# Optimization experiments

Hardware: AMD Instinct MI355X
Metric: run time of the kernel (lower is better)

Reference implementation:

```python
import jax, jax.numpy as jnp
import numpy as np

B, S, D, H, L, V, DF = 2, 1024, 1024, 16, 4, 32000, 4096


def setup_inputs() -> dict:
    key = jax.random.key(0)
    ks = iter(jax.random.split(key, 64))
    rn = lambda shape, s=0.02: jax.random.normal(next(ks), shape, jnp.float32) * s
    inp = {
        'dec_input': rn((B, S, D), 1.0),
        'enc_input': rn((B, S, D), 1.0),
        # additive masks: causal for self-attn, none for cross-attn
        'masked_attention_mask': jnp.where(jnp.tril(jnp.ones((S, S), bool)), 0.0, -1e9)[None, None].astype(jnp.float32),
        'cross_attention_mask': jnp.zeros((1, 1, S, S), jnp.float32),
        'num_heads': H,
    }
    for p in ['sWq', 'sWk', 'sWv', 'sWo', 'cWq', 'cWk', 'cWv', 'cWo']:
        inp[p] = rn((L, D, D))
    for p in ['sbq', 'sbk', 'sbv', 'sbo', 'cbq', 'cbk', 'cbv', 'cbo']:
        inp[p] = jnp.zeros((L, D), jnp.float32)
    for p in ['ln1_g', 'ln2_g', 'ln3_g']:
        inp[p] = jnp.ones((L, D), jnp.float32)
    for p in ['ln1_b', 'ln2_b', 'ln3_b']:
        inp[p] = jnp.zeros((L, D), jnp.float32)
    inp['fW1'] = rn((L, D, DF)); inp['fb1'] = jnp.zeros((L, DF), jnp.float32)
    inp['fW2'] = rn((L, DF, D)); inp['fb2'] = jnp.zeros((L, D), jnp.float32)
    inp['Wout'] = rn((D, V)); inp['bout'] = jnp.zeros((V,), jnp.float32)
    return inp


def positional_encoding(seq_len, d_model, n=10000.0):
    # vectorized equivalent of the original triple-nested loop:
    # even d -> sin(i / n^(d/D)); odd d -> cos(i / n^((d-1)/D)); d==0 denom 1 == n^0
    i = jnp.arange(seq_len, dtype=jnp.float32)[:, None]
    d = jnp.arange(d_model)
    denom = jnp.power(n, (2 * (d // 2)).astype(jnp.float32) / d_model)
    ang = i / denom
    return jnp.where(d % 2 == 0, jnp.sin(ang), jnp.cos(ang))  # [S, D]


def layer_norm(x, g, b, eps=1e-5):
    m = jnp.mean(x, -1, keepdims=True)
    v = jnp.mean(jnp.square(x - m), -1, keepdims=True)
    return (x - m) * jax.lax.rsqrt(v + eps) * g + b


def mha(q_in, k_in, v_in, mask, Wq, bq, Wk, bk, Wv, bv, Wo, bo, h):
    b, sq, d = q_in.shape
    dh = d // h
    q = (q_in @ Wq + bq).reshape(b, sq, h, dh)
    k = (k_in @ Wk + bk).reshape(b, -1, h, dh)
    v = (v_in @ Wv + bv).reshape(b, -1, h, dh)
    scores = jnp.einsum('bqhd,bkhd->bhqk', q, k) / jnp.sqrt(jnp.float32(dh)) + mask
    attn = jax.nn.softmax(scores, axis=-1)
    out = jnp.einsum('bhqk,bkhd->bqhd', attn, v).reshape(b, sq, d)
    return out @ Wo + bo


def reference(dec_input, enc_input, masked_attention_mask, cross_attention_mask,
              sWq, sbq, sWk, sbk, sWv, sbv, sWo, sbo,
              cWq, cbq, cWk, cbk, cWv, cbv, cWo, cbo,
              ln1_g, ln1_b, ln2_g, ln2_b, ln3_g, ln3_b,
              fW1, fb1, fW2, fb2, Wout, bout, num_heads):
    b, s, d = dec_input.shape
    x0 = dec_input + positional_encoding(s, d)
    n_layers = sWq.shape[0]
    y = x0
    for l in range(n_layers):
        # NOTE: original DecoderSequential bug: every block consumes the ORIGINAL input;
        # only the last block's output survives.
        a1 = layer_norm(x0 + mha(x0, x0, x0, masked_attention_mask,
                                 sWq[l], sbq[l], sWk[l], sbk[l], sWv[l], sbv[l], sWo[l], sbo[l], num_heads),
                        ln1_g[l], ln1_b[l])
        a2 = layer_norm(a1 + mha(a1, enc_input, enc_input, cross_attention_mask,
                                 cWq[l], cbq[l], cWk[l], cbk[l], cWv[l], cbv[l], cWo[l], cbo[l], num_heads),
                        ln2_g[l], ln2_b[l])
        ff = jax.nn.relu(a2 @ fW1[l] + fb1[l]) @ fW2[l] + fb2[l]
        y = layer_norm(a2 + ff, ln3_g[l], ln3_b[l])
    return y @ Wout + bout  # [B, S, V]
```

## Files before the change

### kernel.cpp

```cpp
#include <hip/hip_runtime.h>
#include <cstdint>
#include <cstddef>

#define DEV __device__ __forceinline__

typedef __attribute__((ext_vector_type(8))) short short8;
typedef __attribute__((ext_vector_type(4))) float f32x4;
typedef __attribute__((ext_vector_type(16))) float f32x16;
typedef __attribute__((ext_vector_type(4))) unsigned short ushort4v;

DEV unsigned short f2bf(float f){
  union { float f; unsigned int i; } v; v.f = f;
  unsigned int r = v.i + 0x7fffu + ((v.i >> 16) & 1u);
  return (unsigned short)(r >> 16);
}

DEV void gld_lds16(const unsigned short* g, unsigned short* lds){
  __builtin_amdgcn_global_load_lds((const __attribute__((address_space(1))) void*)g,
                                   (__attribute__((address_space(3))) void*)lds, 16, 0, 0);
}

DEV int swz(int r, int s){
  int ln = r >> 1;
  int sl = ((r & 1) << 2) | s;
  return ln * 64 + (((sl ^ (ln & 7))) << 3);
}

template<int BN, int EPI>
__global__ __launch_bounds__(256, 2)
void gemm32(const unsigned short* __restrict__ A,
            const unsigned short* __restrict__ Bt,
            const float* __restrict__ bias,
            void* __restrict__ C, int M, int N, int K)
{
  constexpr int NFR  = BN / 64;
  constexpr int ROWS = 128 + BN;
  constexpr int BUFH = ROWS * 32;
  constexpr int GLD  = ROWS / 64;
  __shared__ __align__(16) unsigned short lds[3 * BUFH];

  const int tid = threadIdx.x, wid = tid >> 6, l = tid & 63;
  const int wr = wid >> 1, wcn = wid & 1;

  const int nbm = M / 128, nbn = N / BN;
  const int nwg = nbm * nbn;
  const int q8 = nwg >> 3, r8 = nwg & 7;
  const int xcd = blockIdx.x & 7, within = blockIdx.x >> 3;
  const int wg = (xcd < r8 ? xcd * (q8 + 1) : r8 * (q8 + 1) + (xcd - r8) * q8) + within;
  const int mb = (wg % nbm) * 128, nb = (wg / nbm) * BN;

  const int nk = K / 32;

  const int sL   = tid >> 3;
  const int sSl  = (tid & 7) ^ (sL & 7);
  const int sRow = sL * 2 + (sSl >> 2);
  const int sKc  = (sSl & 3) * 8;

  const int r31 = l & 31, hi = l >> 5;

  int aoff[2][2], boff[NFR][2];
  #pragma unroll
  for (int m = 0; m < 2; m++)
    #pragma unroll
    for (int ks = 0; ks < 2; ks++)
      aoff[m][ks] = wr * 2048 + swz(m * 32 + r31, 2 * ks + hi);
  #pragma unroll
  for (int n = 0; n < NFR; n++){
    const int col = wcn * (BN / 2) + n * 32 + r31;
    #pragma unroll
    for (int ks = 0; ks < 2; ks++)
      boff[n][ks] = 4096 + (col >> 6) * 2048 + swz(col & 63, 2 * ks + hi);
  }

  f32x16 acc[2][NFR];
  #pragma unroll
  for (int m = 0; m < 2; m++)
    #pragma unroll
    for (int n = 0; n < NFR; n++)
      #pragma unroll
      for (int e = 0; e < 16; e++) acc[m][n][e] = 0.f;

#define STAGE_A(c, tt, b2) \
  gld_lds16(A + (size_t)(mb + (c)*64 + sRow) * K + (size_t)(tt)*32 + sKc, \
            lds + (b2)*BUFH + (c)*2048 + tid*8)
#define STAGE_B(c, tt, b2) \
  gld_lds16(Bt + (size_t)(nb + (c)*64 + sRow) * K + (size_t)(tt)*32 + sKc, \
            lds + (b2)*BUFH + 4096 + (c)*2048 + tid*8)
#define WAIT_GLD() do { if constexpr (GLD == 6) asm volatile("s_waitcnt vmcnt(6)" ::: "memory"); \
                        else if constexpr (GLD == 4) asm volatile("s_waitcnt vmcnt(4)" ::: "memory"); \
                        else asm volatile("s_waitcnt vmcnt(3)" ::: "memory"); } while(0)

  STAGE_A(0, 0, 0); STAGE_A(1, 0, 0);
  #pragma unroll
  for (int c = 0; c < NFR; c++) STAGE_B(c, 0, 0);
  if (nk > 1){
    STAGE_A(0, 1, 1); STAGE_A(1, 1, 1);
    #pragma unroll
    for (int c = 0; c < NFR; c++) STAGE_B(c, 1, 1);
    WAIT_GLD();
  } else {
    asm volatile("s_waitcnt vmcnt(0)" ::: "memory");
  }
  asm volatile("" ::: "memory");
  __builtin_amdgcn_s_barrier();
  asm volatile("" ::: "memory");

  int bb = 0;
  for (int u = 0; u < nk; u++){
    const unsigned short* buf = lds + bb * BUFH;
    const int sb = (bb >= 1) ? bb - 1 : 2;
    const bool st = (u + 2 < nk);
    short8 af[2], bf[NFR];

    af[0] = *(const short8*)(buf + aoff[0][0]);
    af[1] = *(const short8*)(buf + aoff[1][0]);
    #pragma unroll
    for (int n = 0; n < NFR; n++) bf[n] = *(const short8*)(buf + boff[n][0]);
    if (st){
      STAGE_A(0, u + 2, sb); STAGE_A(1, u + 2, sb);
      if constexpr (NFR == 4) STAGE_B(0, u + 2, sb);
    }
    __builtin_amdgcn_s_setprio(1);
    #pragma unroll
    for (int m = 0; m < 2; m++)
      #pragma unroll
      for (int n = 0; n < NFR; n++)
        acc[m][n] = __builtin_amdgcn_mfma_f32_32x32x16_bf16(af[m], bf[n], acc[m][n], 0, 0, 0);
    __builtin_amdgcn_s_setprio(0);

    af[0] = *(const short8*)(buf + aoff[0][1]);
    af[1] = *(const short8*)(buf + aoff[1][1]);
    #pragma unroll
    for (int n = 0; n < NFR; n++) bf[n] = *(const short8*)(buf + boff[n][1]);
    if (st){
      if constexpr (NFR == 4){ STAGE_B(1, u + 2, sb); STAGE_B(2, u + 2, sb); STAGE_B(3, u + 2, sb); }
      else if constexpr (NFR == 2){ STAGE_B(0, u + 2, sb); STAGE_B(1, u + 2, sb); }
      else { STAGE_B(0, u + 2, sb); }
    }
    __builtin_amdgcn_s_setprio(1);
    #pragma unroll
    for (int m = 0; m < 2; m++)
      #pragma unroll
      for (int n = 0; n < NFR; n++)
        acc[m][n] = __builtin_amdgcn_mfma_f32_32x32x16_bf16(af[m], bf[n], acc[m][n], 0, 0, 0);
    __builtin_amdgcn_s_setprio(0);

    if (st)               WAIT_GLD();
    else if (u + 1 < nk)  asm volatile("s_waitcnt vmcnt(0)" ::: "memory");
    asm volatile("" ::: "memory");
    __builtin_amdgcn_s_barrier();
    asm volatile("" ::: "memory");
    bb = (bb == 2) ? 0 : bb + 1;
  }
#undef WAIT_GLD
#undef STAGE_A
#undef STAGE_B

  #pragma unroll
  for (int n = 0; n < NFR; n++){
    const int col = nb + wcn * (BN / 2) + n * 32 + r31;
    const float bv = bias ? bias[col] : 0.f;
    #pragma unroll
    for (int m = 0; m < 2; m++){
      const int rowb = mb + wr * 64 + m * 32 + 4 * hi;
      #pragma unroll
      for (int reg = 0; reg < 16; reg++){
        const int row = rowb + (reg & 3) + 8 * (reg >> 2);
        float v = acc[m][n][reg] + bv;
        size_t idx = (size_t)row * N + col;
        if (EPI == 0)       ((float*)C)[idx] = v;
        else if (EPI == 3)  __builtin_nontemporal_store(v, &((float*)C)[idx]);
        else if (EPI == 1)  ((unsigned short*)C)[idx] = f2bf(v);
        else { v = v > 0.f ? v : 0.f; ((unsigned short*)C)[idx] = f2bf(v); }
      }
    }
  }
}

template<int CAUSAL>
__global__ __launch_bounds__(256)
void attn_kernel(const unsigned short* __restrict__ Qb, int ldq,
                 const unsigned short* __restrict__ Kb, int ldk,
                 const unsigned short* __restrict__ Vb, int ldv,
                 unsigned short* __restrict__ Ob, int ldo)
{
  constexpr int S = 1024;
  __shared__ __align__(16) unsigned short klds[2][4096];
  __shared__ __align__(16) unsigned short vlds[2][4096];
  __shared__ __align__(16) unsigned short plds[4][16][72];

  const int tid = threadIdx.x, w = tid >> 6, l = tid & 63;
  const int qt = blockIdx.x, bh = blockIdx.y;
  const int b = bh >> 4, h = bh & 15;
  const int hoff = h * 64;
  const size_t rb = (size_t)b * S;

  const int qrow = qt * 64 + w * 16 + (l & 15);
  const unsigned short* qp = Qb + (rb + qrow) * ldq + hoff + ((l >> 4) * 8);
  short8 qf0 = *(const short8*)qp;
  short8 qf1 = *(const short8*)(qp + 32);

  float m_run[4] = {-1e30f, -1e30f, -1e30f, -1e30f};
  float l_run[4] = {0.f, 0.f, 0.f, 0.f};
  f32x4 oacc[4];
  #pragma unroll
  for (int t = 0; t < 4; t++) oacc[t] = (f32x4){0.f, 0.f, 0.f, 0.f};

  const int nkv = CAUSAL ? (qt + 1) : (S / 64);

  const int sRowK  = tid >> 3;
  const int sSlotK = (tid & 7) ^ ((tid >> 3) & 7);
  const int skey   = tid >> 3;
  const int sd8    = (tid & 7) * 8;

  int koff[4][2];
  #pragma unroll
  for (int g = 0; g < 4; g++)
    #pragma unroll
    for (int hh = 0; hh < 2; hh++)
      koff[g][hh] = (16 * g + (l & 15)) * 64 + (((hh * 4 + (l >> 4)) ^ (l & 7)) << 3);

  const int vpar = (l >> 3) & 1;
  int voff[4][2];
  #pragma unroll
  for (int t = 0; t < 4; t++)
    #pragma unroll
    for (int ks = 0; ks < 2; ks++)
      voff[t][ks] = (16 * t + (l & 15)) * 64 +
                    ((((ks * 4 + (l >> 4)) ^ (l & 7) ^ ((2 * t + vpar) & 7))) << 3);

#define STAGE_K(c, kt, bf) \
  gld_lds16(Kb + (rb + (size_t)(kt) * 64 + (c) * 32 + sRowK) * ldk + hoff + sSlotK * 8, \
            &klds[bf][(c) * 2048 + tid * 8])
#define LOAD_V(kt, r0v, r1v) do { \
  r0v = *(const short8*)(Vb + (rb + (size_t)(kt) * 64 + skey) * ldv + hoff + sd8); \
  r1v = *(const short8*)(Vb + (rb + (size_t)(kt) * 64 + 32 + skey) * ldv + hoff + sd8); } while(0)
#define WRITE_VT(bf, p, vv) do { \
  _Pragma("unroll") \
  for (int i = 0; i < 8; i++){ \
    vlds[bf][(sd8 + i) * 64 + (((w + 4 * (p)) ^ i ^ (l & 7)) << 3) + (l >> 3)] = \
      (unsigned short)(vv)[i]; \
  } } while(0)

  short8 v0, v1;
  STAGE_K(0, 0, 0); STAGE_K(1, 0, 0);
  LOAD_V(0, v0, v1);
  asm volatile("s_waitcnt vmcnt(0)" ::: "memory");
  WRITE_VT(0, 0, v0); WRITE_VT(0, 1, v1);
  __syncthreads();

  for (int u = 0; u < nkv; u++){
    const int cur = u & 1, nxt = cur ^ 1;
    const bool pre = (u + 1 < nkv);
    if (pre){ STAGE_K(0, u + 1, nxt); STAGE_K(1, u + 1, nxt); LOAD_V(u + 1, v0, v1); }

    f32x4 sc[4];
    #pragma unroll
    for (int g = 0; g < 4; g++){
      short8 k0 = *(const short8*)&klds[cur][koff[g][0]];
      short8 k1 = *(const short8*)&klds[cur][koff[g][1]];
      f32x4 z = (f32x4){0.f, 0.f, 0.f, 0.f};
      z = __builtin_amdgcn_mfma_f32_16x16x32_bf16(qf0, k0, z, 0, 0, 0);
      z = __builtin_amdgcn_mfma_f32_16x16x32_bf16(qf1, k1, z, 0, 0, 0);
      sc[g] = z;
    }

    const bool diag = CAUSAL && (u == qt);
    const int kb = u * 64;
    #pragma unroll
    for (int jj = 0; jj < 4; jj++){
      float s0 = sc[0][jj] * 0.125f, s1 = sc[1][jj] * 0.125f;
      float s2 = sc[2][jj] * 0.125f, s3 = sc[3][jj] * 0.125f;
      if (diag){
        const int q = qt * 64 + w * 16 + ((l >> 4) << 2) + jj;
        const int ky = kb + (l & 15);
        if (ky      > q) s0 = -1e30f;
        if (ky + 16 > q) s1 = -1e30f;
        if (ky + 32 > q) s2 = -1e30f;
        if (ky + 48 > q) s3 = -1e30f;
      }
      float mx = fmaxf(fmaxf(s0, s1), fmaxf(s2, s3));
      mx = fmaxf(mx, __shfl_xor(mx, 1));
      mx = fmaxf(mx, __shfl_xor(mx, 2));
      mx = fmaxf(mx, __shfl_xor(mx, 4));
      mx = fmaxf(mx, __shfl_xor(mx, 8));
      float mnew = fmaxf(m_run[jj], mx);
      float scal = __expf(m_run[jj] - mnew);
      m_run[jj] = mnew;
      float p0 = __expf(s0 - mnew), p1 = __expf(s1 - mnew);
      float p2 = __expf(s2 - mnew), p3 = __expf(s3 - mnew);
      float rs = (p0 + p1) + (p2 + p3);
      rs += __shfl_xor(rs, 1); rs += __shfl_xor(rs, 2);
      rs += __shfl_xor(rs, 4); rs += __shfl_xor(rs, 8);
      l_run[jj] = l_run[jj] * scal + rs;
      #pragma unroll
      for (int t = 0; t < 4; t++) oacc[t][jj] *= scal;
      const int qr = ((l >> 4) << 2) + jj;
      plds[w][qr][l & 15]        = f2bf(p0);
      plds[w][qr][16 + (l & 15)] = f2bf(p1);
      plds[w][qr][32 + (l & 15)] = f2bf(p2);
      plds[w][qr][48 + (l & 15)] = f2bf(p3);
    }
    asm volatile("s_waitcnt lgkmcnt(0)" ::: "memory");
    __builtin_amdgcn_sched_barrier(0);

    short8 pf0 = *(const short8*)&plds[w][l & 15][(l >> 4) * 8];
    short8 pf1 = *(const short8*)&plds[w][l & 15][32 + (l >> 4) * 8];
    #pragma unroll
    for (int t = 0; t < 4; t++){
      short8 va = *(const short8*)&vlds[cur][voff[t][0]];
      short8 vb2 = *(const short8*)&vlds[cur][voff[t][1]];
      f32x4 o = oacc[t];
      o = __builtin_amdgcn_mfma_f32_16x16x32_bf16(pf0, va,  o, 0, 0, 0);
      o = __builtin_amdgcn_mfma_f32_16x16x32_bf16(pf1, vb2, o, 0, 0, 0);
      oacc[t] = o;
    }

    if (pre){
      asm volatile("s_waitcnt vmcnt(0)" ::: "memory");
      WRITE_VT(nxt, 0, v0); WRITE_VT(nxt, 1, v1);
    }
    __syncthreads();
  }
#undef WRITE_VT
#undef LOAD_V
#undef STAGE_K

  #pragma unroll
  for (int jj = 0; jj < 4; jj++){
    float inv = 1.f / l_run[jj];
    int q = qt * 64 + w * 16 + ((l >> 4) << 2) + jj;
    #pragma unroll
    for (int t = 0; t < 4; t++)
      Ob[(rb + q) * ldo + hoff + t * 16 + (l & 15)] = f2bf(oacc[t][jj] * inv);
  }
}

__global__ __launch_bounds__(256)
void ln_kernel(const float* __restrict__ x1, const float* __restrict__ x2,
               const float* __restrict__ g, const float* __restrict__ be,
               float* __restrict__ outf, unsigned short* __restrict__ outb)
{
  const int row = blockIdx.x, t = threadIdx.x;
  __shared__ float red[4];
  const float4 v1 = ((const float4*)(x1 + (size_t)row * 1024))[t];
  const float4 v2 = ((const float4*)(x2 + (size_t)row * 1024))[t];
  float x[4] = {v1.x + v2.x, v1.y + v2.y, v1.z + v2.z, v1.w + v2.w};
  float s = x[0] + x[1] + x[2] + x[3];
  for (int o = 1; o < 64; o <<= 1) s += __shfl_xor(s, o);
  const int w = t >> 6, l = t & 63;
  if (l == 0) red[w] = s;
  __syncthreads();
  const float mean = (red[0] + red[1] + red[2] + red[3]) * (1.f / 1024.f);
  float d[4]; float sq = 0.f;
  #pragma unroll
  for (int i = 0; i < 4; i++){ d[i] = x[i] - mean; sq += d[i] * d[i]; }
  __syncthreads();
  for (int o = 1; o < 64; o <<= 1) sq += __shfl_xor(sq, o);
  if (l == 0) red[w] = sq;
  __syncthreads();
  const float var = (red[0] + red[1] + red[2] + red[3]) * (1.f / 1024.f);
  const float inv = rsqrtf(var + 1e-5f);
  const int base = t * 4;
  #pragma unroll
  for (int i = 0; i < 4; i++){
    float o = d[i] * inv * g[base + i] + be[base + i];
    if (outf) outf[(size_t)row * 1024 + base + i] = o;
    outb[(size_t)row * 1024 + base + i] = f2bf(o);
  }
}

__global__ __launch_bounds__(256)
void build_x0(const float* __restrict__ dec, float* __restrict__ xf, unsigned short* __restrict__ xb)
{
  const int i = blockIdx.x * 256 + threadIdx.x;
  const int i4 = i * 4;
  const int d0 = i4 & 1023;
  const int s  = (i4 >> 10) & 1023;
  float4 dv = ((const float4*)dec)[i];
  const float* dvp = (const float*)&dv;
  float o[4];
  #pragma unroll
  for (int j = 0; j < 4; j++){
    int dd = d0 + j;
    float e = (float)(dd & ~1) * (1.f / 1024.f);
    float den = expf(e * 9.210340371976184f);
    float ang = (float)s / den;
    float pe = (dd & 1) ? cosf(ang) : sinf(ang);
    o[j] = dvp[j] + pe;
  }
  ((float4*)xf)[i] = make_float4(o[0], o[1], o[2], o[3]);
  ushort4v ob; ob[0] = f2bf(o[0]); ob[1] = f2bf(o[1]); ob[2] = f2bf(o[2]); ob[3] = f2bf(o[3]);
  ((ushort4v*)xb)[i] = ob;
}

__global__ __launch_bounds__(256)
void cvt_bf16_k(const float* __restrict__ in, unsigned short* __restrict__ out)
{
  const int i = blockIdx.x * 256 + threadIdx.x;
  float4 v = ((const float4*)in)[i];
  ushort4v o; o[0] = f2bf(v.x); o[1] = f2bf(v.y); o[2] = f2bf(v.z); o[3] = f2bf(v.w);
  ((ushort4v*)out)[i] = o;
}

__global__ __launch_bounds__(256)
void transpose_cvt(const float* __restrict__ in, unsigned short* __restrict__ out, int R, int C)
{
  __shared__ float t[32][65];
  const int cb = blockIdx.x * 32, rb = blockIdx.y * 64;
  const int tx = threadIdx.x & 31, ty = threadIdx.x >> 5;
  #pragma unroll
  for (int i = 0; i < 8; i++)
    t[tx][ty + 8 * i] = in[(size_t)(rb + ty + 8 * i) * C + cb + tx];
  __syncthreads();
  const int lane = threadIdx.x & 63, cr = threadIdx.x >> 6;
  #pragma unroll
  for (int j = 0; j < 8; j++){
    int c = cr + 4 * j;
    out[(size_t)(cb + c) * R + rb + lane] = f2bf(t[c][lane]);
  }
}

struct TPtrs { const float* src[8]; unsigned short* dst[8]; };
__global__ __launch_bounds__(256)
void transpose_cvt8(TPtrs p)
{
  __shared__ float t[32][65];
  const float* __restrict__ in = p.src[blockIdx.z];
  unsigned short* __restrict__ out = p.dst[blockIdx.z];
  const int cb = blockIdx.x * 32, rb = blockIdx.y * 64;
  const int tx = threadIdx.x & 31, ty = threadIdx.x >> 5;
  #pragma unroll
  for (int i = 0; i < 8; i++)
    t[tx][ty + 8 * i] = in[(size_t)(rb + ty + 8 * i) * 1024 + cb + tx];
  __syncthreads();
  const int lane = threadIdx.x & 63, cr = threadIdx.x >> 6;
  #pragma unroll
  for (int j = 0; j < 8; j++){
    int c = cr + 4 * j;
    out[(size_t)(cb + c) * 1024 + rb + lane] = f2bf(t[c][lane]);
  }
}

__global__ __launch_bounds__(256)
void copy_biases(const float* sbq, const float* sbk, const float* sbv,
                 const float* cbk, const float* cbv,
                 float* bqkv, float* bkvc)
{
  const int i = blockIdx.x * 256 + threadIdx.x;
  const int seg = i >> 10, off = i & 1023;
  if (seg == 0)      bqkv[off] = sbq[off];
  else if (seg == 1) bqkv[1024 + off] = sbk[off];
  else if (seg == 2) bqkv[2048 + off] = sbv[off];
  else if (seg == 3) bkvc[off] = cbk[off];
  else               bkvc[1024 + off] = cbv[off];
}

extern "C" void kernel_launch(void* const* d_in, const int* in_sizes, int n_in,
                              void* d_out, int out_size, void* d_ws, size_t ws_size,
                              hipStream_t stream)
{
  constexpr int S = 1024, D = 1024, V = 32000, DF = 4096;
  constexpr int M = 2 * S;
  constexpr int DD = D * D;
  constexpr int l3 = 3;

  const float* dec  = (const float*)d_in[0];
  const float* enc  = (const float*)d_in[1];
  const float* sWq = (const float*)d_in[5]  + l3 * DD;
  const float* sWk = (const float*)d_in[6]  + l3 * DD;
  const float* sWv = (const float*)d_in[7]  + l3 * DD;
  const float* sWo = (const float*)d_in[8]  + l3 * DD;
  const float* cWq = (const float*)d_in[9]  + l3 * DD;
  const float* cWk = (const float*)d_in[10] + l3 * DD;
  const float* cWv = (const float*)d_in[11] + l3 * DD;
  const float* cWo = (const float*)d_in[12] + l3 * DD;
  const float* sbq = (const float*)d_in[13] + l3 * D;
  const float* sbk = (const float*)d_in[14] + l3 * D;
  const float* sbv = (const float*)d_in[15] + l3 * D;
  const float* sbo = (const float*)d_in[16] + l3 * D;
  const float* cbq = (const float*)d_in[17] + l3 * D;
  const float* cbk = (const float*)d_in[18] + l3 * D;
  const float* cbv = (const float*)d_in[19] + l3 * D;
  const float* cbo = (const float*)d_in[20] + l3 * D;
  const float* ln1g = (const float*)d_in[21] + l3 * D;
  const float* ln2g = (const float*)d_in[22] + l3 * D;
  const float* ln3g = (const float*)d_in[23] + l3 * D;
  const float* ln1b = (const float*)d_in[24] + l3 * D;
  const float* ln2b = (const float*)d_in[25] + l3 * D;
  const float* ln3b = (const float*)d_in[26] + l3 * D;
  const float* fW1 = (const float*)d_in[27] + (size_t)l3 * D * DF;
  const float* fb1 = (const float*)d_in[28] + l3 * DF;
  const float* fW2 = (const float*)d_in[29] + (size_t)l3 * DF * D;
  const float* fb2 = (const float*)d_in[30] + l3 * D;
  const float* Wout = (const float*)d_in[31];
  const float* bout = (const float*)d_in[32];
  float* out = (float*)d_out;

  uint8_t* wsp = (uint8_t*)d_ws;
  auto alloc = [&](size_t bytes) -> void* {
    void* p = wsp; wsp += (bytes + 255) & ~(size_t)255; return p;
  };
  float*          x0f  = (float*)alloc((size_t)M * D * 4);
  unsigned short* x0b  = (unsigned short*)alloc((size_t)M * D * 2);
  unsigned short* encb = (unsigned short*)alloc((size_t)M * D * 2);
  unsigned short* wqkv = (unsigned short*)alloc((size_t)3 * DD * 2);
  unsigned short* wos  = (unsigned short*)alloc((size_t)DD * 2);
  unsigned short* wqc  = (unsigned short*)alloc((size_t)DD * 2);
  unsigned short* wkvc = (unsigned short*)alloc((size_t)2 * DD * 2);
  unsigned short* woc  = (unsigned short*)alloc((size_t)DD * 2);
  unsigned short* wf1  = (unsigned short*)alloc((size_t)D * DF * 2);
  unsigned short* wf2  = (unsigned short*)alloc((size_t)D * DF * 2);
  unsigned short* wvo  = (unsigned short*)alloc((size_t)V * D * 2);
  float*          bqkv = (float*)alloc(3 * D * 4);
  float*          bkvc = (float*)alloc(2 * D * 4);
  unsigned short* qkv  = (unsigned short*)alloc((size_t)M * 3 * D * 2);
  unsigned short* attnb= (unsigned short*)alloc((size_t)M * D * 2);
  float*          oproj= (float*)alloc((size_t)M * D * 4);
  float*          a1f  = (float*)alloc((size_t)M * D * 4);
  unsigned short* a1b  = (unsigned short*)alloc((size_t)M * D * 2);
  unsigned short* qc   = (unsigned short*)alloc((size_t)M * D * 2);
  unsigned short* kvc  = (unsigned short*)alloc((size_t)M * 2 * D * 2);
  float*          a2f  = (float*)alloc((size_t)M * D * 4);
  unsigned short* a2b  = (unsigned short*)alloc((size_t)M * D * 2);
  unsigned short* ffh  = (unsigned short*)alloc((size_t)M * DF * 2);
  unsigned short* yb   = (unsigned short*)alloc((size_t)M * D * 2);

  build_x0<<<M * D / 4 / 256, 256, 0, stream>>>(dec, x0f, x0b);
  cvt_bf16_k<<<M * D / 4 / 256, 256, 0, stream>>>(enc, encb);

  TPtrs tp;
  tp.src[0] = sWq; tp.dst[0] = wqkv;
  tp.src[1] = sWk; tp.dst[1] = wqkv + DD;
  tp.src[2] = sWv; tp.dst[2] = wqkv + 2 * DD;
  tp.src[3] = sWo; tp.dst[3] = wos;
  tp.src[4] = cWq; tp.dst[4] = wqc;
  tp.src[5] = cWk; tp.dst[5] = wkvc;
  tp.src[6] = cWv; tp.dst[6] = wkvc + DD;
  tp.src[7] = cWo; tp.dst[7] = woc;
  transpose_cvt8<<<dim3(32, 16, 8), 256, 0, stream>>>(tp);
  transpose_cvt<<<dim3(DF/32, D/64), 256, 0, stream>>>(fW1, wf1, D, DF);
  transpose_cvt<<<dim3(D/32, DF/64), 256, 0, stream>>>(fW2, wf2, DF, D);
  transpose_cvt<<<dim3(V/32, D/64), 256, 0, stream>>>(Wout, wvo, D, V);
  copy_biases<<<20, 256, 0, stream>>>(sbq, sbk, sbv, cbk, cbv, bqkv, bkvc);

  gemm32<128,1><<<(M/128)*(3*D/128), 256, 0, stream>>>(x0b, wqkv, bqkv, qkv, M, 3*D, D);
  attn_kernel<1><<<dim3(S/64, 32), 256, 0, stream>>>(qkv, 3*D, qkv + D, 3*D, qkv + 2*D, 3*D, attnb, D);
  gemm32<64,0><<<(M/128)*(D/64), 256, 0, stream>>>(attnb, wos, sbo, oproj, M, D, D);
  ln_kernel<<<M, 256, 0, stream>>>(x0f, oproj, ln1g, ln1b, a1f, a1b);

  gemm32<64,1><<<(M/128)*(D/64), 256, 0, stream>>>(a1b, wqc, cbq, qc, M, D, D);
  gemm32<128,1><<<(M/128)*(2*D/128), 256, 0, stream>>>(encb, wkvc, bkvc, kvc, M, 2*D, D);
  attn_kernel<0><<<dim3(S/64, 32), 256, 0, stream>>>(qc, D, kvc, 2*D, kvc + D, 2*D, attnb, D);
  gemm32<64,0><<<(M/128)*(D/64), 256, 0, stream>>>(attnb, woc, cbo, oproj, M, D, D);
  ln_kernel<<<M, 256, 0, stream>>>(a1f, oproj, ln2g, ln2b, a2f, a2b);

  gemm32<256,2><<<(M/128)*(DF/256), 256, 0, stream>>>(a2b, wf1, fb1, ffh, M, DF, D);
  gemm32<64,0><<<(M/128)*(D/64), 256, 0, stream>>>(ffh, wf2, fb2, oproj, M, D, DF);
  ln_kernel<<<M, 256, 0, stream>>>(a2f, oproj, ln3g, ln3b, nullptr, yb);

  gemm32<256,3><<<(M/128)*(V/256), 256, 0, stream>>>(yb, wvo, bout, out, M, V, D);
}
```

Baseline: 524.9 us.

## Add 64x128 double-buffered 16x16 MFMA GEMM for mid-size projections

Introduces a new gemm_bt kernel with 64x128 tiles, double-buffered LDS staging via global_load_lds, an XCD-aware workgroup remap, and 16x16x32 bf16 MFMA. It replaces the older gemm32 kernel for the QKV, output, cross-attention and FFN-down projections. The aim is more workgroups and better occupancy (launch bounds 256,2) on the 2048-row GEMMs, which launched few blocks before. The risk is lower arithmetic intensity per tile and a K-step of only 32, which means more frequent syncs.

```diff
diff --git a/kernel.cpp b/kernel.cpp
--- a/kernel.cpp
+++ b/kernel.cpp
@@ -168,6 +168,101 @@
         const int row = rowb + (reg & 3) + 8 * (reg >> 2);
         float v = acc[m][n][reg] + bv;
         size_t idx = (size_t)row * N + col;
+        if (EPI == 0)       ((float*)C)[idx] = v;
+        else if (EPI == 3)  __builtin_nontemporal_store(v, &((float*)C)[idx]);
+        else if (EPI == 1)  ((unsigned short*)C)[idx] = f2bf(v);
+        else { v = v > 0.f ? v : 0.f; ((unsigned short*)C)[idx] = f2bf(v); }
+      }
+    }
+  }
+}
+
+template<int BM, int BN, int EPI>
+__global__ __launch_bounds__(256, 2)
+void gemm_bt(const unsigned short* __restrict__ A,
+             const unsigned short* __restrict__ Bt,
+             const float* __restrict__ bias,
+             void* __restrict__ C, int M, int N, int K)
+{
+  constexpr int MF = BM / 32, NF = BN / 32;
+  constexpr int LA = BM / 64, LB = BN / 64;
+  __shared__ __align__(16) unsigned short lds[2 * (BM + BN) * 32];
+
+  const int tid = threadIdx.x, w = tid >> 6, l = tid & 63;
+  const int wr = w >> 1, wc = w & 1;
+
+  const int nbm = M / BM, nbn = N / BN;
+  const int nwg = nbm * nbn;
+  const int q8 = nwg >> 3, r8 = nwg & 7;
+  const int xcd = blockIdx.x & 7, within = blockIdx.x >> 3;
+  const int wg = (xcd < r8 ? xcd * (q8 + 1) : r8 * (q8 + 1) + (xcd - r8) * q8) + within;
+  const int mb = (wg % nbm) * BM, nb = (wg / nbm) * BN;
+
+  unsigned short* As0 = lds;
+  unsigned short* Bs0 = lds + BM * 32;
+  unsigned short* As1 = lds + (BM + BN) * 32;
+  unsigned short* Bs1 = As1 + BM * 32;
+
+  f32x4 acc[MF][NF];
+  #pragma unroll
+  for (int m = 0; m < MF; m++)
+    #pragma unroll
+    for (int n = 0; n < NF; n++) acc[m][n] = (f32x4){0.f, 0.f, 0.f, 0.f};
+
+  const int srow = l >> 2;
+  const int scol = (((l & 3) ^ ((l >> 2) & 3) ^ ((l >> 4) & 3)) * 8);
+  const int rswz = (l & 3) ^ ((l >> 2) & 3);
+
+  #define STAGE(Ad, Bd, k0) do { \
+    _Pragma("unroll") \
+    for (int i = 0; i < LA; i++){ \
+      int chunk = i * 4 + w; \
+      gld_lds16(A + (size_t)(mb + chunk * 16 + srow) * K + (k0) + scol, (Ad) + chunk * 512); \
+    } \
+    _Pragma("unroll") \
+    for (int i = 0; i < LB; i++){ \
+      int chunk = i * 4 + w; \
+      gld_lds16(Bt + (size_t)(nb + chunk * 16 + srow) * K + (k0) + scol, (Bd) + chunk * 512); \
+    } } while(0)
+
+  STAGE(As0, Bs0, 0);
+  const int nk = K / 32;
+  const int rdoff = ((l >> 4) ^ rswz) * 8;
+  for (int kt = 0; kt < nk; kt++){
+    __syncthreads();
+    unsigned short* Ac = (kt & 1) ? As1 : As0;
+    unsigned short* Bc = (kt & 1) ? Bs1 : Bs0;
+    if (kt + 1 < nk){
+      unsigned short* An = (kt & 1) ? As0 : As1;
+      unsigned short* Bn = (kt & 1) ? Bs0 : Bs1;
+      STAGE(An, Bn, (kt + 1) * 32);
+    }
+    short8 af[MF], bfr[NF];
+    #pragma unroll
+    for (int m = 0; m < MF; m++)
+      af[m] = *(const short8*)(Ac + (wr * (BM / 2) + m * 16 + (l & 15)) * 32 + rdoff);
+    #pragma unroll
+    for (int n = 0; n < NF; n++)
+      bfr[n] = *(const short8*)(Bc + (wc * (BN / 2) + n * 16 + (l & 15)) * 32 + rdoff);
+    #pragma unroll
+    for (int m = 0; m < MF; m++)
+      #pragma unroll
+      for (int n = 0; n < NF; n++)
+        acc[m][n] = __builtin_amdgcn_mfma_f32_16x16x32_bf16(af[m], bfr[n], acc[m][n], 0, 0, 0);
+  }
+  #undef STAGE
+
+  #pragma unroll
+  for (int n = 0; n < NF; n++){
+    const int col = nb + wc * (BN / 2) + n * 16 + (l & 15);
+    const float bv = bias ? bias[col] : 0.f;
+    #pragma unroll
+    for (int m = 0; m < MF; m++){
+      const int row0 = mb + wr * (BM / 2) + m * 16 + ((l >> 4) << 2);
+      #pragma unroll
+      for (int jj = 0; jj < 4; jj++){
+        float v = acc[m][n][jj] + bv;
+        size_t idx = (size_t)(row0 + jj) * N + col;
         if (EPI == 0)       ((float*)C)[idx] = v;
         else if (EPI == 3)  __builtin_nontemporal_store(v, &((float*)C)[idx]);
         else if (EPI == 1)  ((unsigned short*)C)[idx] = f2bf(v);
@@ -544,19 +639,19 @@
   transpose_cvt<<<dim3(V/32, D/64), 256, 0, stream>>>(Wout, wvo, D, V);
   copy_biases<<<20, 256, 0, stream>>>(sbq, sbk, sbv, cbk, cbv, bqkv, bkvc);
 
-  gemm32<128,1><<<(M/128)*(3*D/128), 256, 0, stream>>>(x0b, wqkv, bqkv, qkv, M, 3*D, D);
+  gemm_bt<64,128,1><<<(M/64)*(3*D/128), 256, 0, stream>>>(x0b, wqkv, bqkv, qkv, M, 3*D, D);
   attn_kernel<1><<<dim3(S/64, 32), 256, 0, stream>>>(qkv, 3*D, qkv + D, 3*D, qkv + 2*D, 3*D, attnb, D);
-  gemm32<64,0><<<(M/128)*(D/64), 256, 0, stream>>>(attnb, wos, sbo, oproj, M, D, D);
+  gemm_bt<64,128,0><<<(M/64)*(D/128), 256, 0, stream>>>(attnb, wos, sbo, oproj, M, D, D);
   ln_kernel<<<M, 256, 0, stream>>>(x0f, oproj, ln1g, ln1b, a1f, a1b);
 
-  gemm32<64,1><<<(M/128)*(D/64), 256, 0, stream>>>(a1b, wqc, cbq, qc, M, D, D);
-  gemm32<128,1><<<(M/128)*(2*D/128), 256, 0, stream>>>(encb, wkvc, bkvc, kvc, M, 2*D, D);
+  gemm_bt<64,128,1><<<(M/64)*(D/128), 256, 0, stream>>>(a1b, wqc, cbq, qc, M, D, D);
+  gemm_bt<64,128,1><<<(M/64)*(2*D/128), 256, 0, stream>>>(encb, wkvc, bkvc, kvc, M, 2*D, D);
   attn_kernel<0><<<dim3(S/64, 32), 256, 0, stream>>>(qc, D, kvc, 2*D, kvc + D, 2*D, attnb, D);
-  gemm32<64,0><<<(M/128)*(D/64), 256, 0, stream>>>(attnb, woc, cbo, oproj, M, D, D);
+  gemm_bt<64,128,0><<<(M/64)*(D/128), 256, 0, stream>>>(attnb, woc, cbo, oproj, M, D, D);
   ln_kernel<<<M, 256, 0, stream>>>(a1f, oproj, ln2g, ln2b, a2f, a2b);
 
   gemm32<256,2><<<(M/128)*(DF/256), 256, 0, stream>>>(a2b, wf1, fb1, ffh, M, DF, D);
-  gemm32<64,0><<<(M/128)*(D/64), 256, 0, stream>>>(ffh, wf2, fb2, oproj, M, D, DF);
+  gemm_bt<64,128,0><<<(M/64)*(D/128), 256, 0, stream>>>(ffh, wf2, fb2, oproj, M, D, DF);
   ln_kernel<<<M, 256, 0, stream>>>(a2f, oproj, ln3g, ln3b, nullptr, yb);
 
   gemm32<256,3><<<(M/128)*(V/256), 256, 0, stream>>>(yb, wvo, bout, out, M, V, D);
```

Measured after the change: 550.9 us. +4.9%, slower.

## Add 256x256-tile 512-thread GEMM for vocab projection with XCD-aware block remap

Applied to the files above, without the earlier changes.

Introduces a new GEMM kernel with 256x256 output tiles, 8 waves, BK=64 double-buffered direct-to-LDS loads with swizzle, staggered A/B staging between MFMA phases, and an XCD-aware workgroup index remap. It replaces the 128x256 gemm32 for the large output projection (M=2048, N=32000, K=1024). The intent is higher arithmetic intensity and better L2 locality per XCD for the largest GEMM. The 128 KB of LDS per block and the large accumulator register footprint may limit occupancy, and the epilogue stores are not coalesced.

```diff
diff --git a/kernel.cpp b/kernel.cpp
--- a/kernel.cpp
+++ b/kernel.cpp
@@ -24,6 +24,147 @@
   int ln = r >> 1;
   int sl = ((r & 1) << 2) | s;
   return ln * 64 + (((sl ^ (ln & 7))) << 3);
+}
+
+template<int EPI>
+__global__ __launch_bounds__(512, 2)
+void gemm256(const unsigned short* __restrict__ A,
+             const unsigned short* __restrict__ Bt,
+             const float* __restrict__ bias,
+             void* __restrict__ C, int M, int N, int K)
+{
+  __shared__ __align__(16) unsigned short lds[65536];
+
+  const int tid = threadIdx.x, wid = tid >> 6, l = tid & 63;
+  const int wr = wid >> 2, wc = wid & 3;
+
+  const int nbm = M / 256, nbn = N / 256;
+  const int nwg = nbm * nbn;
+  const int q8 = nwg >> 3, r8 = nwg & 7;
+  const int xcd = blockIdx.x & 7, within = blockIdx.x >> 3;
+  const int wg = (xcd < r8 ? xcd * (q8 + 1) : r8 * (q8 + 1) + (xcd - r8) * q8) + within;
+  const int mb = (wg % nbm) * 256, nb = (wg / nbm) * 256;
+
+  const int nk = K / 64;
+
+  const int srow8 = tid >> 3;
+  const int sslot = (tid & 7) ^ ((tid >> 3) & 7);
+
+  const int rl = l & 15, kslot = l >> 4, sx = l & 7;
+  const int so0 = ((kslot) ^ sx) * 8;
+  const int so1 = ((4 + kslot) ^ sx) * 8;
+  const int arowb = wr * 128 + rl;
+  const int bline = wc * 64 + rl;
+
+  f32x4 acc[8][4];
+  #pragma unroll
+  for (int m = 0; m < 8; m++)
+    #pragma unroll
+    for (int n = 0; n < 4; n++) acc[m][n] = (f32x4){0.f, 0.f, 0.f, 0.f};
+
+#define STAGE_A(c, tt, pp) \
+  gld_lds16(A + (size_t)(mb + (c)*64 + srow8) * K + (size_t)(tt)*64 + sslot*8, \
+            lds + (pp)*32768 + (c)*4096 + tid*8)
+#define STAGE_B(c, tt, pp) \
+  gld_lds16(Bt + (size_t)(nb + (c)*64 + srow8) * K + (size_t)(tt)*64 + sslot*8, \
+            lds + (pp)*32768 + 16384 + (c)*4096 + tid*8)
+
+  STAGE_A(0, 0, 0); STAGE_A(1, 0, 0); STAGE_A(2, 0, 0); STAGE_A(3, 0, 0);
+  STAGE_B(0, 0, 0); STAGE_B(1, 0, 0); STAGE_B(2, 0, 0); STAGE_B(3, 0, 0);
+  if (nk > 1){
+    STAGE_A(0, 1, 1); STAGE_A(1, 1, 1); STAGE_A(2, 1, 1); STAGE_A(3, 1, 1);
+    STAGE_B(0, 1, 1); STAGE_B(1, 1, 1); STAGE_B(2, 1, 1); STAGE_B(3, 1, 1);
+    asm volatile("s_waitcnt vmcnt(8)" ::: "memory");
+  } else {
+    asm volatile("s_waitcnt vmcnt(0)" ::: "memory");
+  }
+  asm volatile("" ::: "memory");
+  __builtin_amdgcn_s_barrier();
+  asm volatile("" ::: "memory");
+
+  for (int u = 0; u < nk; u++){
+    const int pb = u & 1;
+    const unsigned short* buf = lds + pb * 32768;
+    const bool st = (u + 2 < nk);
+    short8 bf[4][2], af[4][2];
+
+    #pragma unroll
+    for (int n = 0; n < 4; n++){
+      const unsigned short* bp = buf + 16384 + (bline + n * 16) * 64;
+      bf[n][0] = *(const short8*)(bp + so0);
+      bf[n][1] = *(const short8*)(bp + so1);
+    }
+    #pragma unroll
+    for (int i = 0; i < 4; i++){
+      const unsigned short* ap = buf + (arowb + i * 16) * 64;
+      af[i][0] = *(const short8*)(ap + so0);
+      af[i][1] = *(const short8*)(ap + so1);
+    }
+    __builtin_amdgcn_s_setprio(1);
+    #pragma unroll
+    for (int i = 0; i < 4; i++)
+      #pragma unroll
+      for (int n = 0; n < 4; n++){
+        acc[i][n] = __builtin_amdgcn_mfma_f32_16x16x32_bf16(af[i][0], bf[n][0], acc[i][n], 0, 0, 0);
+        acc[i][n] = __builtin_amdgcn_mfma_f32_16x16x32_bf16(af[i][1], bf[n][1], acc[i][n], 0, 0, 0);
+      }
+    __builtin_amdgcn_s_setprio(0);
+    asm volatile("" ::: "memory");
+    __builtin_amdgcn_s_barrier();
+    asm volatile("" ::: "memory");
+
+    if (st){ STAGE_B(0, u + 2, pb); STAGE_B(1, u + 2, pb);
+             STAGE_B(2, u + 2, pb); STAGE_B(3, u + 2, pb); }
+
+    #pragma unroll
+    for (int i = 0; i < 4; i++){
+      const unsigned short* ap = buf + (arowb + 64 + i * 16) * 64;
+      af[i][0] = *(const short8*)(ap + so0);
+      af[i][1] = *(const short8*)(ap + so1);
+    }
+    __builtin_amdgcn_s_setprio(1);
+    #pragma unroll
+    for (int i = 0; i < 4; i++)
+      #pragma unroll
+      for (int n = 0; n < 4; n++){
+        acc[4 + i][n] = __builtin_amdgcn_mfma_f32_16x16x32_bf16(af[i][0], bf[n][0], acc[4 + i][n], 0, 0, 0);
+        acc[4 + i][n] = __builtin_amdgcn_mfma_f32_16x16x32_bf16(af[i][1], bf[n][1], acc[4 + i][n], 0, 0, 0);
+      }
+    __builtin_amdgcn_s_setprio(0);
+    asm volatile("" ::: "memory");
+    __builtin_amdgcn_s_barrier();
+    asm volatile("" ::: "memory");
+
+    if (st){ STAGE_A(0, u + 2, pb); STAGE_A(1, u + 2, pb);
+             STAGE_A(2, u + 2, pb); STAGE_A(3, u + 2, pb); }
+
+    if (st)               asm volatile("s_waitcnt vmcnt(8)" ::: "memory");
+    else if (u == nk - 2) asm volatile("s_waitcnt vmcnt(0)" ::: "memory");
+    asm volatile("" ::: "memory");
+    __builtin_amdgcn_s_barrier();
+    asm volatile("" ::: "memory");
+  }
+#undef STAGE_A
+#undef STAGE_B
+
+  #pragma unroll
+  for (int n = 0; n < 4; n++){
+    const int col = nb + wc * 64 + n * 16 + rl;
+    const float bv = bias ? bias[col] : 0.f;
+    #pragma unroll
+    for (int m = 0; m < 8; m++){
+      const int row0 = mb + wr * 128 + m * 16 + (kslot << 2);
+      #pragma unroll
+      for (int jj = 0; jj < 4; jj++){
+        float v = acc[m][n][jj] + bv;
+        size_t idx = (size_t)(row0 + jj) * N + col;
+        if (EPI == 0)       ((float*)C)[idx] = v;
+        else if (EPI == 3)  __builtin_nontemporal_store(v, &((float*)C)[idx]);
+        else if (EPI == 1)  ((unsigned short*)C)[idx] = f2bf(v);
+        else { v = v > 0.f ? v : 0.f; ((unsigned short*)C)[idx] = f2bf(v); }
+      }
+    }
+  }
 }
 
 template<int BN, int EPI>
@@ -559,5 +700,5 @@
   gemm32<64,0><<<(M/128)*(D/64), 256, 0, stream>>>(ffh, wf2, fb2, oproj, M, D, DF);
   ln_kernel<<<M, 256, 0, stream>>>(a2f, oproj, ln3g, ln3b, nullptr, yb);
 
-  gemm32<256,3><<<(M/128)*(V/256), 256, 0, stream>>>(yb, wvo, bout, out, M, V, D);
-}
+  gemm256<3><<<(M/256)*(V/256), 512, 0, stream>>>(yb, wvo, bout, out, M, V, D);
+}
```

After: 528.4 us. About the same (+0.7%).
